# Kernel optimization log

Hardware: AMD Instinct MI355X
Metric: run time of the kernel (lower is better)

Reference implementation:

```python
import jax, jax.numpy as jnp
import numpy as np

N = 50000   # num_nodes
E = 1600000 # edges (avg degree 32)
D = 256     # in_feats
H = 256     # n_hidden


def setup_inputs() -> dict:
    key = jax.random.key(0)
    ks = jax.random.split(key, 9)
    s = 1.0 / np.sqrt(D)
    return {
        "input_nodes": jnp.arange(N, dtype=jnp.int32),
        "edge_src": jax.random.randint(ks[0], (E,), 0, N, dtype=jnp.int32),
        "edge_dst": jax.random.randint(ks[1], (E,), 0, N, dtype=jnp.int32),
        "emb": jax.random.normal(ks[2], (N, D), jnp.float32) * 0.02,
        "W_self0": jax.random.normal(ks[3], (D, H), jnp.float32) * s,
        "W_neigh0": jax.random.normal(ks[4], (D, H), jnp.float32) * s,
        "b0": jnp.zeros((H,), jnp.float32),
        "W_self1": jax.random.normal(ks[5], (H, H), jnp.float32) * s,
        "W_neigh1": jax.random.normal(ks[6], (H, H), jnp.float32) * s,
        "b1": jnp.zeros((H,), jnp.float32),
    }


def _sage_mean(h, src, dst, W_self, W_neigh, b, n):
    # gather neighbor features, mean-reduce by destination, then linear.
    msgs = h[src]                                                  # [E, d]
    ssum = jax.ops.segment_sum(msgs, dst, num_segments=n)          # [n, d]
    deg = jax.ops.segment_sum(jnp.ones(src.shape, h.dtype), dst, num_segments=n)
    h_neigh = ssum / jnp.maximum(deg, 1.0)[:, None]
    return h @ W_self + h_neigh @ W_neigh + b


def reference(input_nodes, edge_src, edge_dst, emb,
              W_self0, W_neigh0, b0, W_self1, W_neigh1, b1):
    h = emb[input_nodes]                                            # [N, D]
    h = _sage_mean(h, edge_src, edge_dst, W_self0, W_neigh0, b0, N)
    h = jax.nn.relu(h)  # dropout is identity at inference
    h = _sage_mean(h, edge_src, edge_dst, W_self1, W_neigh1, b1, N)
    h = h / jnp.linalg.norm(h)  # global Frobenius norm, as in torch.norm(h)
    return h
```

## Files before the change

### kernel.cpp

```cpp
#include <hip/hip_runtime.h>
#include <math.h>

#define NN 50000
#define NE 1600000
#define DF 256
#define NBUCK 391
#define CHS4 ((long long)NN * 64)
#define HALFN 25000

typedef unsigned short ushortT;
typedef __attribute__((ext_vector_type(8))) short short8;
typedef __attribute__((ext_vector_type(4))) float floatx4;
typedef __attribute__((ext_vector_type(4))) unsigned uintx4;

__device__ __forceinline__ unsigned bf16rne(float f) {
    unsigned u = __float_as_uint(f);
    return (u + 0x7fffu + ((u >> 16) & 1u)) >> 16;
}

#define ASYNC16(gptr, ldsptr) \
    __builtin_amdgcn_global_load_lds((const __attribute__((address_space(1))) unsigned*)(gptr), \
                                     (__attribute__((address_space(3))) unsigned*)(ldsptr), 16, 0, 0)


__global__ void k_zero(int* __restrict__ bcnt) {
    int i = blockIdx.x * 256 + threadIdx.x;
    if (i < NBUCK) bcnt[i] = 0;
}

__global__ __launch_bounds__(256)
void k_bhist(const int* __restrict__ dst, int* __restrict__ bcnt) {
    __shared__ int h[NBUCK];
    for (int i = threadIdx.x; i < NBUCK; i += 256) h[i] = 0;
    __syncthreads();
    int base = blockIdx.x * 4096;
#pragma unroll
    for (int i = 0; i < 16; ++i) {
        int e = base + i * 256 + threadIdx.x;
        if (e < NE) atomicAdd(&h[dst[e] >> 7], 1);
    }
    __syncthreads();
    for (int i = threadIdx.x; i < NBUCK; i += 256)
        if (h[i]) atomicAdd(&bcnt[i], h[i]);
}

__global__ void k_bscan(const int* __restrict__ bcnt, int* __restrict__ bbase,
                        int* __restrict__ cursor, int* __restrict__ row_ptr,
                        float* __restrict__ nrm) {
    __shared__ int s[512];
    int t = threadIdx.x;
    int v = (t < NBUCK) ? bcnt[t] : 0;
    s[t] = v; __syncthreads();
    for (int off = 1; off < 512; off <<= 1) {
        int x = (t >= off) ? s[t - off] : 0;
        __syncthreads();
        s[t] += x;
        __syncthreads();
    }
    if (t < NBUCK) { bbase[t] = s[t] - v; cursor[t] = s[t] - v; }
    if (t == 0) { bbase[NBUCK] = NE; row_ptr[NN] = NE; *nrm = 0.0f; }
}

__global__ __launch_bounds__(256)
void k_bin(const int* __restrict__ src, const int* __restrict__ dst,
           int* __restrict__ cursor, unsigned* __restrict__ rec) {
    __shared__ int h[NBUCK];
    __shared__ int gb[NBUCK];
    for (int i = threadIdx.x; i < NBUCK; i += 256) h[i] = 0;
    __syncthreads();
    const int base = blockIdx.x * 2048;
    int bk[8], rk[8];
    unsigned pk[8];
#pragma unroll
    for (int i = 0; i < 8; ++i) {
        int e = base + i * 256 + threadIdx.x;
        if (e < NE) {
            int d = dst[e];
            bk[i] = d >> 7;
            pk[i] = (unsigned)src[e] | ((unsigned)(d & 127) << 16);
            rk[i] = atomicAdd(&h[bk[i]], 1);
        } else bk[i] = -1;
    }
    __syncthreads();
    for (int i = threadIdx.x; i < NBUCK; i += 256) {
        int c = h[i];
        gb[i] = c ? atomicAdd(&cursor[i], c) : 0;
    }
    __syncthreads();
#pragma unroll
    for (int i = 0; i < 8; ++i)
        if (bk[i] >= 0) rec[gb[bk[i]] + rk[i]] = pk[i];
}


__global__ __launch_bounds__(256)
void k_csr(const unsigned* __restrict__ rec, const int* __restrict__ bbase,
           int* __restrict__ row_ptr, ushortT* __restrict__ csr) {
    __shared__ int cnt[256];
    __shared__ int cur[256];
    __shared__ int s[256];
    const int B = blockIdx.x, t = threadIdx.x;
    cnt[t] = 0;
    __syncthreads();
    const int beg = bbase[B], end = bbase[B + 1];
    for (int p = beg + t; p < end; p += 256) {
        unsigned r = rec[p];
        int idx = (int)((r >> 16) & 127) * 2 + ((r & 0xffffu) >= HALFN ? 1 : 0);
        atomicAdd(&cnt[idx], 1);
    }
    __syncthreads();
    int v = cnt[t];
    s[t] = v; __syncthreads();
    for (int off = 1; off < 256; off <<= 1) {
        int x = (t >= off) ? s[t - off] : 0;
        __syncthreads();
        s[t] += x;
        __syncthreads();
    }
    cur[t] = s[t] - v;
    __syncthreads();
    if (t < 128) {
        int node = B * 128 + t;
        if (node < NN) row_ptr[node] = beg + cur[2 * t];
    }
    for (int p = beg + t; p < end; p += 256) {
        unsigned r = rec[p];
        int idx = (int)((r >> 16) & 127) * 2 + ((r & 0xffffu) >= HALFN ? 1 : 0);
        int loc = atomicAdd(&cur[idx], 1);
        csr[beg + loc] = (ushortT)r;
    }
}


__global__ __launch_bounds__(256)
void k_cvt(const float* __restrict__ emb, const int* __restrict__ gather,
           ushortT* __restrict__ embb,
           const float* __restrict__ Ws0, const float* __restrict__ Wn0,
           ushortT* __restrict__ Wt0,
           const float* __restrict__ Ws1, const float* __restrict__ Wn1,
           ushortT* __restrict__ Wt1) {
    const int b = blockIdx.x;
    if (b < 6250) {
        long long i = ((long long)b * 256 + threadIdx.x) * 8;
        int row = (int)(i >> 8);
        int col = (int)(i & 255);
        long long g = (long long)gather[row] * 256 + col;
        float4 v0 = *(const float4*)(emb + g);
        float4 v1 = *(const float4*)(emb + g + 4);
        uint4 o;
        o.x = bf16rne(v0.x) | (bf16rne(v0.y) << 16);
        o.y = bf16rne(v0.z) | (bf16rne(v0.w) << 16);
        o.z = bf16rne(v1.x) | (bf16rne(v1.y) << 16);
        o.w = bf16rne(v1.z) | (bf16rne(v1.w) << 16);
        *(uint4*)(embb + ((long long)(col >> 6) * NN + row) * 64 + (col & 63)) = o;
    } else {
        const bool first = b < 6762;
        const int idx = ((first ? b - 6250 : b - 6762)) * 256 + threadIdx.x;
        const int n = idx >> 9;
        const int k = idx & 511;
        const float* Ws = first ? Ws0 : Ws1;
        const float* Wn = first ? Wn0 : Wn1;
        float v = (k < 256) ? Ws[k * 256 + n] : Wn[(k - 256) * 256 + n];
        (first ? Wt0 : Wt1)[idx] = (ushortT)bf16rne(v);
    }
}


__global__ __launch_bounds__(256)
void k_agg(const ushortT* __restrict__ feat, const int* __restrict__ row_ptr,
           const ushortT* __restrict__ csr, ushortT* __restrict__ out) {
    const int c    = blockIdx.x & 3;
    const int ng   = blockIdx.x >> 2;
    const int node = ng * 32 + (threadIdx.x >> 3);
    const int part = (threadIdx.x & 7) * 8;
    if (node >= NN) return;

    const ushortT* fc = feat + (long long)c * CHS4;
    const int beg = row_ptr[node], end = row_ptr[node + 1];

    float s[8] = {0.f, 0.f, 0.f, 0.f, 0.f, 0.f, 0.f, 0.f};

#define ACCUM(q) do { \
        s[0] += __uint_as_float(q.x << 16); \
        s[1] += __uint_as_float(q.x & 0xffff0000u); \
        s[2] += __uint_as_float(q.y << 16); \
        s[3] += __uint_as_float(q.y & 0xffff0000u); \
        s[4] += __uint_as_float(q.z << 16); \
        s[5] += __uint_as_float(q.z & 0xffff0000u); \
        s[6] += __uint_as_float(q.w << 16); \
        s[7] += __uint_as_float(q.w & 0xffff0000u); \
    } while (0)

    int p = beg;

    if (p < end && (p & 1)) {
        int i0 = (int)__builtin_nontemporal_load(csr + p);
        uintx4 q = *(const uintx4*)(fc + i0 * 64 + part);
        ACCUM(q);
        ++p;
    }

    unsigned x0 = 0, x1 = 0, x2 = 0, x3 = 0;
    if (p + 7 < end) {
        const unsigned* cp = (const unsigned*)(csr + p);
        x0 = __builtin_nontemporal_load(cp + 0);
        x1 = __builtin_nontemporal_load(cp + 1);
        x2 = __builtin_nontemporal_load(cp + 2);
        x3 = __builtin_nontemporal_load(cp + 3);
    }

    while (p + 7 < end) {
        uintx4 q0 = *(const uintx4*)(fc + (int)(x0 & 0xffffu) * 64 + part);
        uintx4 q1 = *(const uintx4*)(fc + (int)(x0 >> 16)     * 64 + part);
        uintx4 q2 = *(const uintx4*)(fc + (int)(x1 & 0xffffu) * 64 + part);
        uintx4 q3 = *(const uintx4*)(fc + (int)(x1 >> 16)     * 64 + part);
        uintx4 q4 = *(const uintx4*)(fc + (int)(x2 & 0xffffu) * 64 + part);
        uintx4 q5 = *(const uintx4*)(fc + (int)(x2 >> 16)     * 64 + part);
        uintx4 q6 = *(const uintx4*)(fc + (int)(x3 & 0xffffu) * 64 + part);
        uintx4 q7 = *(const uintx4*)(fc + (int)(x3 >> 16)     * 64 + part);

        const int np = p + 8;
        if (np + 7 < end) {
            const unsigned* cp = (const unsigned*)(csr + np);
            x0 = __builtin_nontemporal_load(cp + 0);
            x1 = __builtin_nontemporal_load(cp + 1);
            x2 = __builtin_nontemporal_load(cp + 2);
            x3 = __builtin_nontemporal_load(cp + 3);
        }

        ACCUM(q0); ACCUM(q1); ACCUM(q2); ACCUM(q3);
        ACCUM(q4); ACCUM(q5); ACCUM(q6); ACCUM(q7);
        p = np;
    }

    for (; p < end; ++p) {
        int i0 = (int)__builtin_nontemporal_load(csr + p);
        uintx4 q = *(const uintx4*)(fc + i0 * 64 + part);
        ACCUM(q);
    }
#undef ACCUM

    float inv = 1.0f / fmaxf((float)(end - beg), 1.0f);
    uintx4 o;
    o.x = bf16rne(s[0] * inv) | (bf16rne(s[1] * inv) << 16);
    o.y = bf16rne(s[2] * inv) | (bf16rne(s[3] * inv) << 16);
    o.z = bf16rne(s[4] * inv) | (bf16rne(s[5] * inv) << 16);
    o.w = bf16rne(s[6] * inv) | (bf16rne(s[7] * inv) << 16);
    __builtin_nontemporal_store(o, (uintx4*)(out + ((long long)c * NN + node) * 64 + part));
}


template<int RELU, int NORM>
__global__ __launch_bounds__(256, 4)
void k_gemm(const ushortT* __restrict__ Aself, const ushortT* __restrict__ Aneigh,
            const ushortT* __restrict__ Wt, const float* __restrict__ bias,
            ushortT* __restrict__ Cb, float* __restrict__ Cf, float* __restrict__ norm_acc) {
    __shared__ ushortT As[2048];
    __shared__ ushortT Bs[8192];
    __shared__ float red[4];

    const int t = threadIdx.x;
    const int w = t >> 6;
    const int lane = t & 63;
    const int m0 = blockIdx.x * 64;

    const int ar = t >> 2;
    const int cu = (t & 3) * 8;

    const long long gA = (long long)min(m0 + ar, NN - 1) * 64 + cu;

    const unsigned ldsA = w * 512;
    const unsigned ldsB = w * 512;

    const int fm = lane & 15;
    const int fk = (lane >> 4) * 8;

    floatx4 acc[4][4];
#pragma unroll
    for (int i = 0; i < 4; ++i)
#pragma unroll
        for (int j = 0; j < 4; ++j) acc[i][j] = (floatx4){0.f, 0.f, 0.f, 0.f};

    for (int kt = 0; kt < 512; kt += 32) {
        const int kc = (kt < 256) ? kt : kt - 256;
        const ushortT* Ab = ((kt < 256) ? Aself : Aneigh)
                          + (long long)(kc >> 6) * CHS4 + (kc & 32);

        __syncthreads();
        ASYNC16(Ab + gA, As + ldsA);
#pragma unroll
        for (int i = 0; i < 4; ++i)
            ASYNC16(Wt + (i * 64 + ar) * 512 + kt + cu, Bs + i * 2048 + ldsB);
        __syncthreads();

        short8 af[4], bf[4];
#pragma unroll
        for (int i = 0; i < 4; ++i)
            af[i] = *(const short8*)&As[(i * 16 + fm) * 32 + fk];
#pragma unroll
        for (int j = 0; j < 4; ++j)
            bf[j] = *(const short8*)&Bs[(w * 64 + j * 16 + fm) * 32 + fk];
#pragma unroll
        for (int i = 0; i < 4; ++i)
#pragma unroll
            for (int j = 0; j < 4; ++j)
                acc[i][j] = __builtin_amdgcn_mfma_f32_16x16x32_bf16(af[i], bf[j], acc[i][j], 0, 0, 0);
    }

    float bj[4];
#pragma unroll
    for (int j = 0; j < 4; ++j) bj[j] = bias[w * 64 + j * 16 + fm];

    float sumsq = 0.0f;
#pragma unroll
    for (int i = 0; i < 4; ++i) {
#pragma unroll
        for (int r = 0; r < 4; ++r) {
            const int row = m0 + i * 16 + (lane >> 4) * 4 + r;
            if (row < NN) {
#pragma unroll
                for (int j = 0; j < 4; ++j) {
                    const int col = w * 64 + j * 16 + fm;
                    float v = acc[i][j][r] + bj[j];
                    if (RELU) v = fmaxf(v, 0.0f);
                    if (NORM) {
                        Cf[(long long)row * 256 + col] = v;
                        sumsq += v * v;
                    } else {
                        Cb[((long long)(col >> 6) * NN + row) * 64 + (col & 63)] = (ushortT)bf16rne(v);
                    }
                }
            }
        }
    }

    if (NORM) {
#pragma unroll
        for (int off = 32; off > 0; off >>= 1) sumsq += __shfl_down(sumsq, off);
        if (lane == 0) red[w] = sumsq;
        __syncthreads();
        if (t == 0) atomicAdd(norm_acc, red[0] + red[1] + red[2] + red[3]);
    }
}

__global__ void k_scale(float* __restrict__ out, const float* __restrict__ nrm) {
    const float s = 1.0f / sqrtf(*nrm);
    long long i = ((long long)blockIdx.x * 256 + threadIdx.x) * 4;
    float4 v = *(float4*)&out[i];
    v.x *= s; v.y *= s; v.z *= s; v.w *= s;
    *(float4*)&out[i] = v;
}


extern "C" void kernel_launch(void* const* d_in, const int* in_sizes, int n_in,
                              void* d_out, int out_size, void* d_ws, size_t ws_size,
                              hipStream_t stream) {
    const int*   input_nodes = (const int*)d_in[0];
    const int*   esrc = (const int*)d_in[1];
    const int*   edst = (const int*)d_in[2];
    const float* emb  = (const float*)d_in[3];
    const float* Ws0  = (const float*)d_in[4];
    const float* Wn0  = (const float*)d_in[5];
    const float* b0   = (const float*)d_in[6];
    const float* Ws1  = (const float*)d_in[7];
    const float* Wn1  = (const float*)d_in[8];
    const float* b1   = (const float*)d_in[9];
    float* out = (float*)d_out;

    char* base = (char*)d_ws;
    ushortT*  embb    = (ushortT*) (base);
    ushortT*  h1b     = (ushortT*) (base + 25600000);
    ushortT*  hnb     = (ushortT*) (base + 51200000);
    unsigned* rec     = (unsigned*)(base + 76800000);
    ushortT*  csr     = (ushortT*) (base + 83200000);
    ushortT*  Wt0     = (ushortT*) (base + 86400000);
    ushortT*  Wt1     = (ushortT*) (base + 86662144);
    int*      row_ptr = (int*)     (base + 86924288);
    int*      bcnt    = (int*)     (base + 87124304);
    int*      bbase   = (int*)     (base + 87125904);
    int*      cursor  = (int*)     (base + 87127504);
    float*    nrm     = (float*)   (base + 87129104);

    k_zero  <<<2,     256, 0, stream>>>(bcnt);
    k_bhist <<<391,   256, 0, stream>>>(edst, bcnt);
    k_bscan <<<1,     512, 0, stream>>>(bcnt, bbase, cursor, row_ptr, nrm);
    k_bin   <<<782,   256, 0, stream>>>(esrc, edst, cursor, rec);
    k_csr   <<<NBUCK, 256, 0, stream>>>(rec, bbase, row_ptr, csr);

    k_cvt<<<7274, 256, 0, stream>>>(emb, input_nodes, embb, Ws0, Wn0, Wt0, Ws1, Wn1, Wt1);

    const int GEMM_BLOCKS = (NN + 63) / 64;
    const int AGG_BLOCKS  = ((NN + 31) / 32) * 4;

    k_agg<<<AGG_BLOCKS, 256, 0, stream>>>(embb, row_ptr, csr, hnb);
    k_gemm<1, 0><<<GEMM_BLOCKS, 256, 0, stream>>>(embb, hnb, Wt0, b0, h1b, nullptr, nullptr);

    k_agg<<<AGG_BLOCKS, 256, 0, stream>>>(h1b, row_ptr, csr, hnb);
    k_gemm<0, 1><<<GEMM_BLOCKS, 256, 0, stream>>>(h1b, hnb, Wt1, b1, nullptr, out, nrm);

    k_scale<<<NN * DF / 4 / 256, 256, 0, stream>>>(out, nrm);
}
```

Baseline: 453.8 us.

## Split neighbor aggregation into two passes by source-node half for cache locality

The CSR build now records, per destination node, where the edges from sources in the upper half of the node range begin. Each aggregation is split into two kernel launches: the first sums only neighbours from the lower half and writes a bf16 partial, and the second sums the upper half, adds the partial, and applies the mean. This keeps the gathered feature working set per pass to about half the table so it fits better in cache. The cost is an extra launch, an extra bf16 round-trip of the partial sums (which adds rounding error), and reading row pointers twice.

```diff
diff --git a/kernel.cpp b/kernel.cpp
--- a/kernel.cpp
+++ b/kernel.cpp
@@ -95,7 +95,7 @@
 
 __global__ __launch_bounds__(256)
 void k_csr(const unsigned* __restrict__ rec, const int* __restrict__ bbase,
-           int* __restrict__ row_ptr, ushortT* __restrict__ csr) {
+           int* __restrict__ row_ptr, int* __restrict__ hp, ushortT* __restrict__ csr) {
     __shared__ int cnt[256];
     __shared__ int cur[256];
     __shared__ int s[256];
@@ -121,7 +121,10 @@
     __syncthreads();
     if (t < 128) {
         int node = B * 128 + t;
-        if (node < NN) row_ptr[node] = beg + cur[2 * t];
+        if (node < NN) {
+            row_ptr[node] = beg + s[2 * t] - cnt[2 * t];
+            hp[node]      = beg + s[2 * t + 1] - cnt[2 * t + 1];
+        }
     }
     for (int p = beg + t; p < end; p += 256) {
         unsigned r = rec[p];
@@ -166,9 +169,11 @@
 }
 
 
+template<int PHASE>
 __global__ __launch_bounds__(256)
 void k_agg(const ushortT* __restrict__ feat, const int* __restrict__ row_ptr,
-           const ushortT* __restrict__ csr, ushortT* __restrict__ out) {
+           const int* __restrict__ hp, const ushortT* __restrict__ csr,
+           const ushortT* __restrict__ pin, ushortT* __restrict__ out) {
     const int c    = blockIdx.x & 3;
     const int ng   = blockIdx.x >> 2;
     const int node = ng * 32 + (threadIdx.x >> 3);
@@ -176,7 +181,11 @@
     if (node >= NN) return;
 
     const ushortT* fc = feat + (long long)c * CHS4;
-    const int beg = row_ptr[node], end = row_ptr[node + 1];
+    const int rbeg = row_ptr[node];
+    const int rend = row_ptr[node + 1];
+    const int hb   = hp[node];
+    int p        = (PHASE == 0) ? rbeg : hb;
+    const int hi = (PHASE == 0) ? hb   : rend;
 
     float s[8] = {0.f, 0.f, 0.f, 0.f, 0.f, 0.f, 0.f, 0.f};
 
@@ -191,9 +200,7 @@
         s[7] += __uint_as_float(q.w & 0xffff0000u); \
     } while (0)
 
-    int p = beg;
-
-    if (p < end && (p & 1)) {
+    if (p < hi && (p & 1)) {
         int i0 = (int)__builtin_nontemporal_load(csr + p);
         uintx4 q = *(const uintx4*)(fc + i0 * 64 + part);
         ACCUM(q);
@@ -201,7 +208,7 @@
     }
 
     unsigned x0 = 0, x1 = 0, x2 = 0, x3 = 0;
-    if (p + 7 < end) {
+    if (p + 7 < hi) {
         const unsigned* cp = (const unsigned*)(csr + p);
         x0 = __builtin_nontemporal_load(cp + 0);
         x1 = __builtin_nontemporal_load(cp + 1);
@@ -209,7 +216,7 @@
         x3 = __builtin_nontemporal_load(cp + 3);
     }
 
-    while (p + 7 < end) {
+    while (p + 7 < hi) {
         uintx4 q0 = *(const uintx4*)(fc + (int)(x0 & 0xffffu) * 64 + part);
         uintx4 q1 = *(const uintx4*)(fc + (int)(x0 >> 16)     * 64 + part);
         uintx4 q2 = *(const uintx4*)(fc + (int)(x1 & 0xffffu) * 64 + part);
@@ -220,7 +227,7 @@
         uintx4 q7 = *(const uintx4*)(fc + (int)(x3 >> 16)     * 64 + part);
 
         const int np = p + 8;
-        if (np + 7 < end) {
+        if (np + 7 < hi) {
             const unsigned* cp = (const unsigned*)(csr + np);
             x0 = __builtin_nontemporal_load(cp + 0);
             x1 = __builtin_nontemporal_load(cp + 1);
@@ -233,20 +240,30 @@
         p = np;
     }
 
-    for (; p < end; ++p) {
+    for (; p < hi; ++p) {
         int i0 = (int)__builtin_nontemporal_load(csr + p);
         uintx4 q = *(const uintx4*)(fc + i0 * 64 + part);
         ACCUM(q);
     }
+
+    const long long oaddr = ((long long)c * NN + node) * 64 + part;
+    uintx4 o;
+    if (PHASE == 0) {
+        o.x = bf16rne(s[0]) | (bf16rne(s[1]) << 16);
+        o.y = bf16rne(s[2]) | (bf16rne(s[3]) << 16);
+        o.z = bf16rne(s[4]) | (bf16rne(s[5]) << 16);
+        o.w = bf16rne(s[6]) | (bf16rne(s[7]) << 16);
+    } else {
+        uintx4 q = __builtin_nontemporal_load((const uintx4*)(pin + oaddr));
+        ACCUM(q);
+        float inv = 1.0f / fmaxf((float)(rend - rbeg), 1.0f);
+        o.x = bf16rne(s[0] * inv) | (bf16rne(s[1] * inv) << 16);
+        o.y = bf16rne(s[2] * inv) | (bf16rne(s[3] * inv) << 16);
+        o.z = bf16rne(s[4] * inv) | (bf16rne(s[5] * inv) << 16);
+        o.w = bf16rne(s[6] * inv) | (bf16rne(s[7] * inv) << 16);
+    }
 #undef ACCUM
-
-    float inv = 1.0f / fmaxf((float)(end - beg), 1.0f);
-    uintx4 o;
-    o.x = bf16rne(s[0] * inv) | (bf16rne(s[1] * inv) << 16);
-    o.y = bf16rne(s[2] * inv) | (bf16rne(s[3] * inv) << 16);
-    o.z = bf16rne(s[4] * inv) | (bf16rne(s[5] * inv) << 16);
-    o.w = bf16rne(s[6] * inv) | (bf16rne(s[7] * inv) << 16);
-    __builtin_nontemporal_store(o, (uintx4*)(out + ((long long)c * NN + node) * 64 + part));
+    __builtin_nontemporal_store(o, (uintx4*)(out + oaddr));
 }
 
 
@@ -376,26 +393,29 @@
     ushortT*  Wt0     = (ushortT*) (base + 86400000);
     ushortT*  Wt1     = (ushortT*) (base + 86662144);
     int*      row_ptr = (int*)     (base + 86924288);
-    int*      bcnt    = (int*)     (base + 87124304);
-    int*      bbase   = (int*)     (base + 87125904);
-    int*      cursor  = (int*)     (base + 87127504);
-    float*    nrm     = (float*)   (base + 87129104);
+    int*      hp      = (int*)     (base + 87124304);
+    int*      bcnt    = (int*)     (base + 87324304);
+    int*      bbase   = (int*)     (base + 87325904);
+    int*      cursor  = (int*)     (base + 87327504);
+    float*    nrm     = (float*)   (base + 87329104);
 
     k_zero  <<<2,     256, 0, stream>>>(bcnt);
     k_bhist <<<391,   256, 0, stream>>>(edst, bcnt);
     k_bscan <<<1,     512, 0, stream>>>(bcnt, bbase, cursor, row_ptr, nrm);
     k_bin   <<<782,   256, 0, stream>>>(esrc, edst, cursor, rec);
-    k_csr   <<<NBUCK, 256, 0, stream>>>(rec, bbase, row_ptr, csr);
+    k_csr   <<<NBUCK, 256, 0, stream>>>(rec, bbase, row_ptr, hp, csr);
 
     k_cvt<<<7274, 256, 0, stream>>>(emb, input_nodes, embb, Ws0, Wn0, Wt0, Ws1, Wn1, Wt1);
 
     const int GEMM_BLOCKS = (NN + 63) / 64;
     const int AGG_BLOCKS  = ((NN + 31) / 32) * 4;
 
-    k_agg<<<AGG_BLOCKS, 256, 0, stream>>>(embb, row_ptr, csr, hnb);
+    k_agg<0><<<AGG_BLOCKS, 256, 0, stream>>>(embb, row_ptr, hp, csr, nullptr, h1b);
+    k_agg<1><<<AGG_BLOCKS, 256, 0, stream>>>(embb, row_ptr, hp, csr, h1b, hnb);
     k_gemm<1, 0><<<GEMM_BLOCKS, 256, 0, stream>>>(embb, hnb, Wt0, b0, h1b, nullptr, nullptr);
 
-    k_agg<<<AGG_BLOCKS, 256, 0, stream>>>(h1b, row_ptr, csr, hnb);
+    k_agg<0><<<AGG_BLOCKS, 256, 0, stream>>>(h1b, row_ptr, hp, csr, nullptr, embb);
+    k_agg<1><<<AGG_BLOCKS, 256, 0, stream>>>(h1b, row_ptr, hp, csr, embb, hnb);
     k_gemm<0, 1><<<GEMM_BLOCKS, 256, 0, stream>>>(h1b, hnb, Wt1, b1, nullptr, out, nrm);
 
     k_scale<<<NN * DF / 4 / 256, 256, 0, stream>>>(out, nrm);
```

Measured after the change: 504.3 us. 1.11x slower.
